# Kernel tuning notes

Measured on AMD Instinct MI355X. Metric: run time of the kernel, lower is better.

Reference implementation:

```python
import jax, jax.numpy as jnp
import numpy as np

B, F, D, A = 1024, 33, 128, 128  # batch, num_fields, embed_dim, attn_size (A must equal gnn dim)

def setup_inputs() -> dict:
    key = jax.random.key(0)
    k1, k2, k3, k4 = jax.random.split(key, 4)
    gnn_feature = jax.random.normal(k1, (B, A), dtype=jnp.float32)
    x = jax.random.normal(k2, (B, F, D), dtype=jnp.float32)
    # attention Linear(embed_dim -> attn_size): weight (A, D), bias (A,)
    lim = 1.0 / np.sqrt(D)
    attn_W = jax.random.uniform(k3, (A, D), minval=-lim, maxval=lim, dtype=jnp.float32)
    attn_b = jax.random.uniform(k4, (A,), minval=-lim, maxval=lim, dtype=jnp.float32)
    return {"gnn_feature": gnn_feature, "x": x, "attn_W": attn_W, "attn_b": attn_b}

def reference(gnn_feature, x, attn_W, attn_b):
    num_fields = x.shape[1]
    row, col = np.triu_indices(num_fields, k=1)  # P = F*(F-1)/2 pairs
    inner = x[:, row] * x[:, col]                # [B, P, D]
    fm = jax.nn.relu(jnp.einsum('bpd,ad->bpa', inner, attn_W) + attn_b)  # [B, P, A]
    # bmm(gnn[b,1,A], fm[b,p,A,1]) -> dot product per pair, softmax over pairs
    scores = jnp.einsum('ba,bpa->bp', gnn_feature, fm)  # [B, P]
    attn = jax.nn.softmax(scores, axis=1)               # [B, P]
    attn_output = jnp.einsum('bp,bpd->bd', attn, inner) * 100.0  # [B, D]
    return jnp.concatenate([gnn_feature, attn_output], axis=1)   # [B, A+D]
```

## Files before the change

### kernel.cpp

```cpp
#include <hip/hip_runtime.h>
#include <hip/hip_bf16.h>

#define FN 33
#define DN 128
#define AN 128
#define PN 528
#define MTN 33
#define XS 136
#define TS 36

typedef __attribute__((ext_vector_type(8))) short short8;
typedef __attribute__((ext_vector_type(4))) float f32x4;
typedef __attribute__((ext_vector_type(4))) int i32x4;

union V4 { i32x4 i; short8 s; f32x4 f; };

__device__ __forceinline__ float bitf(unsigned int u) { return __builtin_bit_cast(float, u); }
__device__ __forceinline__ unsigned int fbits(float f) { return __builtin_bit_cast(unsigned int, f); }

__device__ __forceinline__ unsigned int pack2_bf16(float lo, float hi) {
  unsigned int ul = fbits(lo) + 0x8000u;
  unsigned int uh = fbits(hi) + 0x8000u;
  return __builtin_amdgcn_perm(uh, ul, 0x07060302);
}

__global__ __launch_bounds__(256, 2)
void afm_kernel(const float* __restrict__ gnn, const float* __restrict__ xg,
                const float* __restrict__ Wg,  const float* __restrict__ bg,
                float* __restrict__ out)
{
  __shared__ __align__(16) unsigned short Wl[AN * XS];
  __shared__ __align__(16) unsigned short xb[FN * XS];
  __shared__ __align__(16) float xT[DN * TS];
  __shared__ __align__(16) float attn2d[FN * TS];
  __shared__ __align__(16) float scores_s[PN];
  __shared__ float gnn_s[AN];
  __shared__ float bias_s[AN];
  __shared__ unsigned short rowcol[PN];
  __shared__ float red[8];

  const int tid  = threadIdx.x;
  const int b    = blockIdx.x;
  const int wave = tid >> 6;
  const int lane = tid & 63;
  const int q    = lane >> 4;
  const int u    = lane & 15;

  for (int idx = tid; idx < FN * TS; idx += 256) attn2d[idx] = 0.0f;

  const f32x4* xg4 = (const f32x4*)(xg + (size_t)b * FN * DN);
  for (int idx = tid; idx < (FN * DN) / 4; idx += 256) {
    f32x4 v = xg4[idx];
    int i  = idx >> 5;
    int d0 = (idx & 31) << 2;
    unsigned int lo = pack2_bf16(v.x, v.y);
    unsigned int hi = pack2_bf16(v.z, v.w);
    *(uint2*)&xb[i * XS + d0] = make_uint2(lo, hi);
    xT[(d0 + 0) * TS + i] = v.x;
    xT[(d0 + 1) * TS + i] = v.y;
    xT[(d0 + 2) * TS + i] = v.z;
    xT[(d0 + 3) * TS + i] = v.w;
  }
  if (tid < DN) {
    xT[tid * TS + 33] = 0.f; xT[tid * TS + 34] = 0.f; xT[tid * TS + 35] = 0.f;
  }

  const f32x4* Wg4 = (const f32x4*)Wg;
  for (int idx = tid; idx < (AN * DN) / 4; idx += 256) {
    f32x4 v = Wg4[idx];
    int a  = idx >> 5;
    int d0 = (idx & 31) << 2;
    *(uint2*)&Wl[a * XS + d0] = make_uint2(pack2_bf16(v.x, v.y), pack2_bf16(v.z, v.w));
  }
  if (tid < AN) {
    gnn_s[tid]  = gnn[(size_t)b * AN + tid];
    bias_s[tid] = bg[tid];
  }
  for (int p = tid; p < PN; p += 256) {
    int i = 0, rem = p;
    while (rem >= FN - 1 - i) { rem -= FN - 1 - i; i++; }
    rowcol[p] = (unsigned short)(i | ((i + 1 + rem) << 8));
  }
  __syncthreads();

  V4 Bf[8][4];
  #pragma unroll
  for (int n = 0; n < 8; n++)
    #pragma unroll
    for (int kk = 0; kk < 4; kk++)
      Bf[n][kk].i = *(const i32x4*)&Wl[(n * 16 + u) * XS + kk * 32 + q * 8];

  float garr[8], barr[8];
  #pragma unroll
  for (int n = 0; n < 8; n++) { garr[n] = gnn_s[n * 16 + u]; barr[n] = bias_s[n * 16 + u]; }

  for (int mt = wave; mt < MTN; mt += 4) {
    const int p = mt * 16 + u;
    const unsigned int rc = rowcol[p];
    const int r = rc & 255, c = rc >> 8;

    V4 Af[4];
    #pragma unroll
    for (int kk = 0; kk < 4; kk++) {
      i32x4 xr = *(const i32x4*)&xb[r * XS + kk * 32 + q * 8];
      i32x4 xc = *(const i32x4*)&xb[c * XS + kk * 32 + q * 8];
      i32x4 o;
      #pragma unroll
      for (int t = 0; t < 4; t++) {
        unsigned int ar = (unsigned int)xr[t], ac = (unsigned int)xc[t];
        float flo = bitf(ar << 16) * bitf(ac << 16);
        float fhi = bitf(ar & 0xffff0000u) * bitf(ac & 0xffff0000u);
        o[t] = (int)pack2_bf16(flo, fhi);
      }
      Af[kk].i = o;
    }

    f32x4 acc[8];
    #pragma unroll
    for (int n = 0; n < 8; n++) acc[n] = (f32x4){0.f, 0.f, 0.f, 0.f};
    #pragma unroll
    for (int kk = 0; kk < 4; kk++)
      #pragma unroll
      for (int n = 0; n < 8; n++)
        acc[n] = __builtin_amdgcn_mfma_f32_16x16x32_bf16(Af[kk].s, Bf[n][kk].s, acc[n], 0, 0, 0);

    float sc[4] = {0.f, 0.f, 0.f, 0.f};
    #pragma unroll
    for (int n = 0; n < 8; n++)
      #pragma unroll
      for (int rr = 0; rr < 4; rr++) {
        float fmv = acc[n][rr] + barr[n];
        fmv = fmv > 0.f ? fmv : 0.f;
        sc[rr] = fmaf(fmv, garr[n], sc[rr]);
      }
    #pragma unroll
    for (int off = 1; off < 16; off <<= 1)
      #pragma unroll
      for (int rr = 0; rr < 4; rr++)
        sc[rr] += __shfl_xor(sc[rr], off, 64);
    if (u == 0)
      *(f32x4*)&scores_s[mt * 16 + q * 4] = (f32x4){sc[0], sc[1], sc[2], sc[3]};
  }
  __syncthreads();

  float s0 = scores_s[tid];
  float s1 = scores_s[tid + 256];
  float s2 = (tid < 16) ? scores_s[tid + 512] : -3.4e38f;
  float m = fmaxf(fmaxf(s0, s1), s2);
  #pragma unroll
  for (int off = 32; off >= 1; off >>= 1) m = fmaxf(m, __shfl_xor(m, off, 64));
  if (lane == 0) red[wave] = m;
  __syncthreads();
  const float smax = fmaxf(fmaxf(red[0], red[1]), fmaxf(red[2], red[3]));

  float e0 = __expf(s0 - smax);
  float e1 = __expf(s1 - smax);
  float e2 = (tid < 16) ? __expf(s2 - smax) : 0.f;
  {
    unsigned int rc = rowcol[tid];
    attn2d[(rc & 255) * TS + ((rc >> 8) - (rc & 255) - 1)] = e0;
    rc = rowcol[tid + 256];
    attn2d[(rc & 255) * TS + ((rc >> 8) - (rc & 255) - 1)] = e1;
    if (tid < 16) {
      rc = rowcol[tid + 512];
      attn2d[(rc & 255) * TS + ((rc >> 8) - (rc & 255) - 1)] = e2;
    }
  }
  float lsum = e0 + e1 + e2;
  #pragma unroll
  for (int off = 32; off >= 1; off >>= 1) lsum += __shfl_xor(lsum, off, 64);
  if (lane == 0) red[4 + wave] = lsum;
  __syncthreads();
  const float Z = red[4] + red[5] + red[6] + red[7];

  if (tid < DN) {
    const int d = tid;
    float xcol[36];
    #pragma unroll
    for (int t = 0; t < 9; t++) {
      f32x4 v = *(const f32x4*)&xT[d * TS + t * 4];
      xcol[t * 4 + 0] = v.x; xcol[t * 4 + 1] = v.y;
      xcol[t * 4 + 2] = v.z; xcol[t * 4 + 3] = v.w;
    }
    float acc = 0.f;
    #pragma unroll
    for (int i = 0; i < FN - 1; i++) {
      const int L = FN - 1 - i;
      const int nf4 = (L + 3) >> 2;
      float ti = 0.f;
      #pragma unroll
      for (int t = 0; t < nf4; t++) {
        f32x4 a4 = *(const f32x4*)&attn2d[i * TS + t * 4];
        ti = fmaf(a4.x, xcol[i + 1 + t * 4 + 0], ti);
        ti = fmaf(a4.y, xcol[i + 1 + t * 4 + 1], ti);
        ti = fmaf(a4.z, xcol[i + 1 + t * 4 + 2], ti);
        ti = fmaf(a4.w, xcol[i + 1 + t * 4 + 3], ti);
      }
      acc = fmaf(xcol[i], ti, acc);
    }
    out[(size_t)b * (AN + DN) + AN + d] = acc * (100.0f / Z);
  } else {
    const int a = tid - 128;
    out[(size_t)b * (AN + DN) + a] = gnn_s[a];
  }
}

extern "C" void kernel_launch(void* const* d_in, const int* in_sizes, int n_in,
                              void* d_out, int out_size, void* d_ws, size_t ws_size,
                              hipStream_t stream) {
  (void)n_in; (void)out_size; (void)d_ws; (void)ws_size;
  const float* gnn  = (const float*)d_in[0];
  const float* x    = (const float*)d_in[1];
  const float* W    = (const float*)d_in[2];
  const float* bias = (const float*)d_in[3];
  float* out = (float*)d_out;
  const int Bn = in_sizes[0] / AN;
  afm_kernel<<<dim3(Bn), dim3(256), 0, stream>>>(gnn, x, W, bias, out);
}
```

Measured before the change: 117.3 us.

## Switch to fp16 MFMA, load W directly to registers, split final reduction

Replaces bf16 emulation with fp16 packing (cvt_pkrtz) and native half8 multiplies feeding the f16 MFMA. Drops the per-block shared staging of W, gnn, bias and the fp32 transposed x copy, loading W straight from global into registers and reading x columns from the fp16 shared buffer. Swaps shuffle-based row sums for DPP row reductions and splits the final weighted sum across all 256 threads with a shared partial-sum buffer. This shrinks shared memory and instruction count but changes numerics (fp16 range and rounding, and the output reduction now uses fp16-rounded x) and issues uncoalesced per-lane global reads of W.

```diff
diff --git a/kernel.cpp b/kernel.cpp
--- a/kernel.cpp
+++ b/kernel.cpp
@@ -1,5 +1,4 @@
 #include <hip/hip_runtime.h>
-#include <hip/hip_bf16.h>
 
 #define FN 33
 #define DN 128
@@ -9,19 +8,19 @@
 #define XS 136
 #define TS 36
 
-typedef __attribute__((ext_vector_type(8))) short short8;
+typedef __attribute__((ext_vector_type(8))) _Float16 half8;
 typedef __attribute__((ext_vector_type(4))) float f32x4;
-typedef __attribute__((ext_vector_type(4))) int i32x4;
-
-union V4 { i32x4 i; short8 s; f32x4 f; };
-
-__device__ __forceinline__ float bitf(unsigned int u) { return __builtin_bit_cast(float, u); }
-__device__ __forceinline__ unsigned int fbits(float f) { return __builtin_bit_cast(unsigned int, f); }
-
-__device__ __forceinline__ unsigned int pack2_bf16(float lo, float hi) {
-  unsigned int ul = fbits(lo) + 0x8000u;
-  unsigned int uh = fbits(hi) + 0x8000u;
-  return __builtin_amdgcn_perm(uh, ul, 0x07060302);
+
+__device__ __forceinline__ unsigned int pkrtz(float a, float b) {
+  return __builtin_bit_cast(unsigned int, __builtin_amdgcn_cvt_pkrtz(a, b));
+}
+
+__device__ __forceinline__ float row_sum16(float v) {
+  v += __builtin_bit_cast(float, __builtin_amdgcn_update_dpp(0, __builtin_bit_cast(int, v), 0x128, 0xF, 0xF, false));
+  v += __builtin_bit_cast(float, __builtin_amdgcn_update_dpp(0, __builtin_bit_cast(int, v), 0x124, 0xF, 0xF, false));
+  v += __builtin_bit_cast(float, __builtin_amdgcn_update_dpp(0, __builtin_bit_cast(int, v), 0x122, 0xF, 0xF, false));
+  v += __builtin_bit_cast(float, __builtin_amdgcn_update_dpp(0, __builtin_bit_cast(int, v), 0x121, 0xF, 0xF, false));
+  return v;
 }
 
 __global__ __launch_bounds__(256, 2)
@@ -29,13 +28,10 @@
                 const float* __restrict__ Wg,  const float* __restrict__ bg,
                 float* __restrict__ out)
 {
-  __shared__ __align__(16) unsigned short Wl[AN * XS];
-  __shared__ __align__(16) unsigned short xb[FN * XS];
-  __shared__ __align__(16) float xT[DN * TS];
+  __shared__ __align__(16) _Float16 xh[FN * XS];
   __shared__ __align__(16) float attn2d[FN * TS];
   __shared__ __align__(16) float scores_s[PN];
-  __shared__ float gnn_s[AN];
-  __shared__ float bias_s[AN];
+  __shared__ __align__(16) float part[256];
   __shared__ unsigned short rowcol[PN];
   __shared__ float red[8];
 
@@ -53,66 +49,49 @@
     f32x4 v = xg4[idx];
     int i  = idx >> 5;
     int d0 = (idx & 31) << 2;
-    unsigned int lo = pack2_bf16(v.x, v.y);
-    unsigned int hi = pack2_bf16(v.z, v.w);
-    *(uint2*)&xb[i * XS + d0] = make_uint2(lo, hi);
-    xT[(d0 + 0) * TS + i] = v.x;
-    xT[(d0 + 1) * TS + i] = v.y;
-    xT[(d0 + 2) * TS + i] = v.z;
-    xT[(d0 + 3) * TS + i] = v.w;
-  }
-  if (tid < DN) {
-    xT[tid * TS + 33] = 0.f; xT[tid * TS + 34] = 0.f; xT[tid * TS + 35] = 0.f;
-  }
-
-  const f32x4* Wg4 = (const f32x4*)Wg;
-  for (int idx = tid; idx < (AN * DN) / 4; idx += 256) {
-    f32x4 v = Wg4[idx];
-    int a  = idx >> 5;
-    int d0 = (idx & 31) << 2;
-    *(uint2*)&Wl[a * XS + d0] = make_uint2(pack2_bf16(v.x, v.y), pack2_bf16(v.z, v.w));
-  }
-  if (tid < AN) {
-    gnn_s[tid]  = gnn[(size_t)b * AN + tid];
-    bias_s[tid] = bg[tid];
+    *(uint2*)&xh[i * XS + d0] = make_uint2(pkrtz(v.x, v.y), pkrtz(v.z, v.w));
   }
   for (int p = tid; p < PN; p += 256) {
     int i = 0, rem = p;
     while (rem >= FN - 1 - i) { rem -= FN - 1 - i; i++; }
     rowcol[p] = (unsigned short)(i | ((i + 1 + rem) << 8));
   }
-  __syncthreads();
-
-  V4 Bf[8][4];
-  #pragma unroll
-  for (int n = 0; n < 8; n++)
-    #pragma unroll
-    for (int kk = 0; kk < 4; kk++)
-      Bf[n][kk].i = *(const i32x4*)&Wl[(n * 16 + u) * XS + kk * 32 + q * 8];
-
+
+  half8 Bf[8][4];
+  #pragma unroll
+  for (int n = 0; n < 8; n++) {
+    const float* wrow = Wg + (size_t)(n * 16 + u) * DN + q * 8;
+    #pragma unroll
+    for (int kk = 0; kk < 4; kk++) {
+      f32x4 w0 = *(const f32x4*)(wrow + kk * 32);
+      f32x4 w1 = *(const f32x4*)(wrow + kk * 32 + 4);
+      union { half8 h; unsigned int w[4]; } t;
+      t.w[0] = pkrtz(w0.x, w0.y);
+      t.w[1] = pkrtz(w0.z, w0.w);
+      t.w[2] = pkrtz(w1.x, w1.y);
+      t.w[3] = pkrtz(w1.z, w1.w);
+      Bf[n][kk] = t.h;
+    }
+  }
   float garr[8], barr[8];
   #pragma unroll
-  for (int n = 0; n < 8; n++) { garr[n] = gnn_s[n * 16 + u]; barr[n] = bias_s[n * 16 + u]; }
+  for (int n = 0; n < 8; n++) {
+    garr[n] = gnn[(size_t)b * AN + n * 16 + u];
+    barr[n] = bg[n * 16 + u];
+  }
+  __syncthreads();
 
   for (int mt = wave; mt < MTN; mt += 4) {
     const int p = mt * 16 + u;
     const unsigned int rc = rowcol[p];
     const int r = rc & 255, c = rc >> 8;
 
-    V4 Af[4];
+    half8 Af[4];
     #pragma unroll
     for (int kk = 0; kk < 4; kk++) {
-      i32x4 xr = *(const i32x4*)&xb[r * XS + kk * 32 + q * 8];
-      i32x4 xc = *(const i32x4*)&xb[c * XS + kk * 32 + q * 8];
-      i32x4 o;
-      #pragma unroll
-      for (int t = 0; t < 4; t++) {
-        unsigned int ar = (unsigned int)xr[t], ac = (unsigned int)xc[t];
-        float flo = bitf(ar << 16) * bitf(ac << 16);
-        float fhi = bitf(ar & 0xffff0000u) * bitf(ac & 0xffff0000u);
-        o[t] = (int)pack2_bf16(flo, fhi);
-      }
-      Af[kk].i = o;
+      half8 xr = *(const half8*)&xh[r * XS + kk * 32 + q * 8];
+      half8 xc = *(const half8*)&xh[c * XS + kk * 32 + q * 8];
+      Af[kk] = xr * xc;
     }
 
     f32x4 acc[8];
@@ -122,7 +101,7 @@
     for (int kk = 0; kk < 4; kk++)
       #pragma unroll
       for (int n = 0; n < 8; n++)
-        acc[n] = __builtin_amdgcn_mfma_f32_16x16x32_bf16(Af[kk].s, Bf[n][kk].s, acc[n], 0, 0, 0);
+        acc[n] = __builtin_amdgcn_mfma_f32_16x16x32_f16(Af[kk], Bf[n][kk], acc[n], 0, 0, 0);
 
     float sc[4] = {0.f, 0.f, 0.f, 0.f};
     #pragma unroll
@@ -134,10 +113,7 @@
         sc[rr] = fmaf(fmv, garr[n], sc[rr]);
       }
     #pragma unroll
-    for (int off = 1; off < 16; off <<= 1)
-      #pragma unroll
-      for (int rr = 0; rr < 4; rr++)
-        sc[rr] += __shfl_xor(sc[rr], off, 64);
+    for (int rr = 0; rr < 4; rr++) sc[rr] = row_sum16(sc[rr]);
     if (u == 0)
       *(f32x4*)&scores_s[mt * 16 + q * 4] = (f32x4){sc[0], sc[1], sc[2], sc[3]};
   }
@@ -173,23 +149,25 @@
   __syncthreads();
   const float Z = red[4] + red[5] + red[6] + red[7];
 
-  if (tid < DN) {
-    const int d = tid;
+  {
+    const int d = tid & 127;
+    const int h = tid >> 7;
     float xcol[36];
     #pragma unroll
-    for (int t = 0; t < 9; t++) {
-      f32x4 v = *(const f32x4*)&xT[d * TS + t * 4];
-      xcol[t * 4 + 0] = v.x; xcol[t * 4 + 1] = v.y;
-      xcol[t * 4 + 2] = v.z; xcol[t * 4 + 3] = v.w;
-    }
+    for (int i = 0; i < FN; i++) xcol[i] = (float)xh[i * XS + d];
+    xcol[33] = 0.f; xcol[34] = 0.f; xcol[35] = 0.f;
+
     float acc = 0.f;
-    #pragma unroll
-    for (int i = 0; i < FN - 1; i++) {
+    const int ibeg = h * 16, iend = ibeg + 16;
+    #pragma unroll
+    for (int i = 0; i < 32; i++) {
+      if (i < ibeg || i >= iend) continue;
       const int L = FN - 1 - i;
       const int nf4 = (L + 3) >> 2;
       float ti = 0.f;
       #pragma unroll
-      for (int t = 0; t < nf4; t++) {
+      for (int t = 0; t < 8; t++) {
+        if (t >= nf4) break;
         f32x4 a4 = *(const f32x4*)&attn2d[i * TS + t * 4];
         ti = fmaf(a4.x, xcol[i + 1 + t * 4 + 0], ti);
         ti = fmaf(a4.y, xcol[i + 1 + t * 4 + 1], ti);
@@ -198,10 +176,15 @@
       }
       acc = fmaf(xcol[i], ti, acc);
     }
-    out[(size_t)b * (AN + DN) + AN + d] = acc * (100.0f / Z);
+    part[tid] = acc;
+  }
+  __syncthreads();
+  if (tid < DN) {
+    float tot = part[tid] + part[tid + 128];
+    out[(size_t)b * (AN + DN) + AN + tid] = tot * (100.0f / Z);
   } else {
     const int a = tid - 128;
-    out[(size_t)b * (AN + DN) + a] = gnn_s[a];
+    out[(size_t)b * (AN + DN) + a] = gnn[(size_t)b * AN + a];
   }
 }
 
```

Result: no change. 116.5 us (-0.6%).
